# Kernel tuning notes

Measured on AMD Instinct MI355X. Metric: run time of the kernel, lower is better.

Reference implementation:

```python
import jax, jax.numpy as jnp
import numpy as np

EMBED_DIM = 1024
N_HEADS = 16
HEAD_DIM = EMBED_DIM // N_HEADS


def setup_inputs() -> dict:
    key = jax.random.key(0)
    k1, k2, k3 = jax.random.split(key, 3)
    B, T, C = 2, 2048, EMBED_DIM
    x = jax.random.normal(k1, (B, T, C), dtype=jnp.float32)
    # nn.Linear-style init scale
    s = 1.0 / np.sqrt(C)
    Wqkv = jax.random.normal(k2, (C, 3 * C), dtype=jnp.float32) * s
    bqkv = jnp.zeros((3 * C,), dtype=jnp.float32)
    Wout = jax.random.normal(k3, (C, C), dtype=jnp.float32) * s
    bout = jnp.zeros((C,), dtype=jnp.float32)
    return {"x": x, "Wqkv": Wqkv, "bqkv": bqkv, "Wout": Wout, "bout": bout}


def reference(x, Wqkv, bqkv, Wout, bout):
    B, T, C = x.shape
    H, D = N_HEADS, HEAD_DIM
    qkv = x @ Wqkv + bqkv  # [B,T,3C]
    q, k, v = jnp.split(qkv, 3, axis=-1)
    # [B,T,C] -> [B,H,T,D]
    q = q.reshape(B, T, H, D).transpose(0, 2, 1, 3)
    k = k.reshape(B, T, H, D).transpose(0, 2, 1, 3)
    v = v.reshape(B, T, H, D).transpose(0, 2, 1, 3)
    scale = 1.0 / np.sqrt(D)
    scores = jnp.einsum("bhqd,bhkd->bhqk", q, k) * scale  # [B,H,T,T]
    causal = jnp.tril(jnp.ones((T, T), dtype=bool))  # True where allowed
    scores = jnp.where(causal, scores, jnp.finfo(scores.dtype).min)
    attn = jax.nn.softmax(scores, axis=-1)
    out = jnp.einsum("bhqk,bhkd->bhqd", attn, v)  # [B,H,T,D]
    out = out.transpose(0, 2, 1, 3).reshape(B, T, C)
    return out @ Wout + bout
```

## Files before the change

kernel.cpp:

```cpp
#include <hip/hip_runtime.h>
#include <hip/hip_bf16.h>
#include <stdint.h>

#define EMBED 1024
#define NH 16
#define HD 64
#define BATCH 2
#define SEQ 2048
#define MTOK (BATCH*SEQ)

using bf8 = __attribute__((ext_vector_type(8))) short;
using f4  = __attribute__((ext_vector_type(4))) float;
using f16v = __attribute__((ext_vector_type(16))) float;
using u16x4 = __attribute__((ext_vector_type(4))) unsigned short;

union U4 { uint32_t u[4]; bf8 v; };

__device__ __forceinline__ uint32_t pk_bf16(float a, float b) {
  __hip_bfloat162 h = __float22bfloat162_rn(float2{a, b});
  union { __hip_bfloat162 h; uint32_t u; } c; c.h = h; return c.u;
}
__device__ __forceinline__ unsigned short bfbits(float f) {
  __hip_bfloat16 h = __float2bfloat16(f);
  union { __hip_bfloat16 h; unsigned short u; } c; c.h = h; return c.u;
}
__device__ __forceinline__ float bf2f(unsigned short u) {
  union { uint32_t u; float f; } c; c.u = (uint32_t)u << 16; return c.f;
}
__device__ __forceinline__ float fexp2(float x) {
#if __has_builtin(__builtin_amdgcn_exp2f)
  return __builtin_amdgcn_exp2f(x);
#else
  return exp2f(x);
#endif
}
__device__ __forceinline__ float frcp(float x) {
#if __has_builtin(__builtin_amdgcn_rcpf)
  return __builtin_amdgcn_rcpf(x);
#else
  return 1.f / x;
#endif
}

__device__ __forceinline__ void gl2lds16(const void* g, void* l) {
  __builtin_amdgcn_global_load_lds(
      (const __attribute__((address_space(1))) void*)g,
      (__attribute__((address_space(3))) void*)l, 16, 0, 0);
}

__global__ __launch_bounds__(256) void prep(const float* __restrict__ x,
                                            unsigned short* __restrict__ xb,
                                            const float* __restrict__ Wqkv,
                                            unsigned short* __restrict__ wqkvT,
                                            const float* __restrict__ Wout,
                                            unsigned short* __restrict__ woutT) {
  __shared__ float tl[64][65];
  int blk = blockIdx.x;
  if (blk < 4096) {
    int i = (blk * 256 + threadIdx.x) * 4;
    float4 v = *(const float4*)(x + i);
    uint2 o;
    o.x = pk_bf16(v.x, v.y);
    o.y = pk_bf16(v.z, v.w);
    *(uint2*)(xb + i) = o;
    return;
  }
  const float* W; unsigned short* Wt; int K, N, bx, by;
  if (blk < 4096 + 768) {
    int j = blk - 4096; W = Wqkv; Wt = wqkvT; K = 1024; N = 3072;
    bx = j % 48; by = j / 48;
  } else {
    int j = blk - 4096 - 768; W = Wout; Wt = woutT; K = 1024; N = 1024;
    bx = j % 16; by = j / 16;
  }
  int k0 = by * 64, n0 = bx * 64;
  int tr = threadIdx.x >> 6, tc = threadIdx.x & 63;
#pragma unroll
  for (int i = 0; i < 16; i++) {
    int r = tr + i * 4;
    tl[r][tc] = W[(size_t)(k0 + r) * N + n0 + tc];
  }
  __syncthreads();
#pragma unroll
  for (int i = 0; i < 16; i++) {
    int r = tr + i * 4;
    Wt[(size_t)(n0 + r) * K + k0 + tc] = bfbits(tl[tc][r]);
  }
}

template<int BN, int MODE>
__global__ __launch_bounds__(256) void gemm_bt(const unsigned short* __restrict__ A,
                                               const unsigned short* __restrict__ Bt,
                                               const float* __restrict__ bias,
                                               unsigned short* __restrict__ Oq,
                                               unsigned short* __restrict__ Ov,
                                               float* __restrict__ Of,
                                               int M, int N, int K) {
  constexpr int MT = (BN == 128) ? 4 : 2;
  constexpr int BB = BN * 128;
  const int tid = threadIdx.x;
  const int w = tid >> 6, lane = tid & 63;
  const int wm = (BN == 128) ? (w >> 1) : w;
  const int wn = (BN == 128) ? (w & 1) : 0;
  const int m0 = blockIdx.y * 128, n0 = blockIdx.x * BN;

  __shared__ char smem[32768 + 2 * BB];

  f4 acc[MT][4] = {};

  auto STAGE = [&](int buf, int kk) {
    int k0 = kk * 64;
#pragma unroll
    for (int i = 0; i < 4; i++) {
      int c = i * 4 + w;
      int row = c * 8 + (lane >> 3);
      int col = ((lane & 7) * 8) ^ ((row & 7) << 3);
      gl2lds16(A + (size_t)(m0 + row) * K + k0 + col, smem + buf * 16384 + c * 1024);
    }
#pragma unroll
    for (int i = 0; i < BN / 32; i++) {
      int c = i * 4 + w;
      int row = c * 8 + (lane >> 3);
      int col = ((lane & 7) * 8) ^ ((row & 7) << 3);
      gl2lds16(Bt + (size_t)(n0 + row) * K + k0 + col, smem + 32768 + buf * BB + c * 1024);
    }
  };

  const int nk = K / 64;
  STAGE(0, 0);
  STAGE(1, 1);

  for (int kk = 0; kk < nk; kk++) {
    if (kk + 1 < nk) {
      if constexpr (BN == 128) { asm volatile("s_waitcnt vmcnt(8)" ::: "memory"); }
      else                     { asm volatile("s_waitcnt vmcnt(6)" ::: "memory"); }
    } else {
      asm volatile("s_waitcnt vmcnt(0)" ::: "memory");
    }
    __builtin_amdgcn_s_barrier();

    const char* Al = smem + (kk & 1) * 16384;
    const char* Bl = smem + 32768 + (kk & 1) * BB;
    __builtin_amdgcn_s_setprio(1);
#pragma unroll
    for (int ks = 0; ks < 2; ks++) {
      bf8 af[MT], bfr[4];
#pragma unroll
      for (int mt = 0; mt < MT; mt++) {
        int rr = wm * (MT * 16) + mt * 16 + (lane & 15);
        af[mt] = *(const bf8*)(Al + rr * 128 + ((ks * 64 + (lane >> 4) * 16) ^ ((rr & 7) << 4)));
      }
#pragma unroll
      for (int nt = 0; nt < 4; nt++) {
        int rr = wn * 64 + nt * 16 + (lane & 15);
        bfr[nt] = *(const bf8*)(Bl + rr * 128 + ((ks * 64 + (lane >> 4) * 16) ^ ((rr & 7) << 4)));
      }
#pragma unroll
      for (int mt = 0; mt < MT; mt++)
#pragma unroll
        for (int nt = 0; nt < 4; nt++)
          acc[mt][nt] = __builtin_amdgcn_mfma_f32_16x16x32_bf16(af[mt], bfr[nt], acc[mt][nt], 0, 0, 0);
    }
    __builtin_amdgcn_s_setprio(0);

    __builtin_amdgcn_s_barrier();
    if (kk + 2 < nk) STAGE(kk & 1, kk + 2);
  }

  if (MODE == 0) {
    const int region = n0 >> 10;
    if (region < 2) {
      float sc = (region == 0) ? 0.180336880f : 1.0f;
#pragma unroll
      for (int nt = 0; nt < 4; nt++) {
        int n = n0 + wn * 64 + nt * 16 + (lane & 15);
        float bv = bias[n];
        int c = n & 1023, h = c >> 6, d = c & 63;
#pragma unroll
        for (int mt = 0; mt < MT; mt++) {
#pragma unroll
          for (int r = 0; r < 4; r++) {
            int m = m0 + wm * (MT * 16) + mt * 16 + (lane >> 4) * 4 + r;
            int b = m >> 11, t = m & 2047;
            size_t off = ((((size_t)region * 2 + b) * 16 + h) * 2048 + t) * 64 + d;
            Oq[off] = bfbits((acc[mt][nt][r] + bv) * sc);
          }
        }
      }
    } else {
#pragma unroll
      for (int nt = 0; nt < 4; nt++) {
        int n = n0 + wn * 64 + nt * 16 + (lane & 15);
        float bv = bias[n];
        int c = n & 1023, h = c >> 6, d = c & 63;
#pragma unroll
        for (int mt = 0; mt < MT; mt++) {
          int m = m0 + wm * (MT * 16) + mt * 16 + (lane >> 4) * 4;
          int b = m >> 11, t = m & 2047;
          size_t off = (((size_t)b * 16 + h) * 64 + d) * 2048 + t;
          u16x4 pk4;
#pragma unroll
          for (int r = 0; r < 4; r++) pk4[r] = bfbits(acc[mt][nt][r] + bv);
          *(u16x4*)(Ov + off) = pk4;
        }
      }
    }
  } else {
#pragma unroll
    for (int mt = 0; mt < MT; mt++) {
#pragma unroll
      for (int r = 0; r < 4; r++) {
        int m = m0 + wm * (MT * 16) + mt * 16 + (lane >> 4) * 4 + r;
#pragma unroll
        for (int nt = 0; nt < 4; nt++) {
          int n = n0 + wn * 64 + nt * 16 + (lane & 15);
          Of[(size_t)m * N + n] = acc[mt][nt][r] + bias[n];
        }
      }
    }
  }
}

__global__ __launch_bounds__(256) void attn12(const unsigned short* __restrict__ Qb,
                                              const unsigned short* __restrict__ Kb,
                                              const unsigned short* __restrict__ Vtb,
                                              unsigned short* __restrict__ Ob,
                                              unsigned short* __restrict__ partO,
                                              float* __restrict__ Lbuf) {
  static const signed char QTs[32] = {15,15,14,14,13,13,12,12,11,11,10,10,9,8,7,6,5,15,4,9,14,3,8,13,2,7,12,1,6,11,0,5};
  static const signed char TSs[32] = {0,11,0,11,0,11,0,11,0,11,0,11,0,0,0,0,0,22,0,11,22,0,11,22,0,11,22,0,11,22,0,11};
  static const signed char PS[32]  = {0,1,2,3,4,5,6,7,8,9,10,11,12,13,14,15,16,17,-1,18,19,-1,20,21,-1,22,23,-1,24,25,-1,26};
  const int idx = blockIdx.x;
  const int s = idx >> 5, bh = idx & 31;
  const int qt = QTs[s], ts = TSs[s];
  const int ntot = 2 * qt + 2;
  const int te = min(ts + 11, ntot);
  const int slot = PS[s];

  const int tid = threadIdx.x;
  const int w = tid >> 6, lane = tid & 63;
  const int hi = lane >> 5, q32 = lane & 31;

  __shared__ char smem[49152];

  const unsigned short* Qg  = Qb  + (size_t)bh * SEQ * HD;
  const unsigned short* Kg  = Kb  + (size_t)bh * SEQ * HD;
  const unsigned short* Vtg = Vtb + (size_t)bh * SEQ * HD;

  const int qbw  = qt * 128 + w * 32;
  const int qrow = qbw + q32;

  bf8 qf[4];
#pragma unroll
  for (int kc = 0; kc < 4; kc++)
    qf[kc] = *(const bf8*)(Qg + (size_t)qrow * HD + kc * 16 + hi * 8);

  f16v acc0 = {}, acc1 = {};
  float lr = 0.f;

  auto STAGE = [&](int buf, int t) {
    int kv0 = t * 64;
#pragma unroll
    for (int i = 0; i < 2; i++) {
      int c = i * 4 + w;
      int row = c * 8 + (lane >> 3);
      int col = ((lane & 7) * 8) ^ ((row & 7) << 3);
      gl2lds16(Kg + (size_t)(kv0 + row) * HD + col,    smem + buf * 8192 + c * 1024);
      gl2lds16(Vtg + (size_t)row * SEQ + kv0 + col,    smem + 24576 + buf * 8192 + c * 1024);
    }
  };

  const int nt_loc = te - ts;
  STAGE(0, ts);
  if (nt_loc > 1) STAGE(1, ts + 1);

  for (int tl = 0; tl < nt_loc; tl++) {
    const int t = ts + tl;
    const int kv0 = t * 64;

    if (tl + 1 < nt_loc) {
      asm volatile("s_waitcnt vmcnt(4)" ::: "memory");
    } else {
      asm volatile("s_waitcnt vmcnt(0)" ::: "memory");
    }
    __builtin_amdgcn_s_barrier();
    if (tl + 2 < nt_loc) STAGE((tl + 2) % 3, t + 2);

    if (kv0 <= qbw + 31) {
      const char* kl = smem + (tl % 3) * 8192;
      const char* vl = smem + 24576 + (tl % 3) * 8192;
      const bool hi_vis = (kv0 + 32 <= qbw + 31);

      f16v s0 = {}, s1 = {};
      __builtin_amdgcn_s_setprio(1);
#pragma unroll
      for (int kc = 0; kc < 4; kc++) {
        int r0 = q32;
        bf8 k0 = *(const bf8*)(kl + r0 * 128 + ((kc * 32 + hi * 16) ^ ((r0 & 7) << 4)));
        s0 = __builtin_amdgcn_mfma_f32_32x32x16_bf16(k0, qf[kc], s0, 0, 0, 0);
      }
      if (hi_vis) {
#pragma unroll
        for (int kc = 0; kc < 4; kc++) {
          int r1 = 32 + q32;
          bf8 k1 = *(const bf8*)(kl + r1 * 128 + ((kc * 32 + hi * 16) ^ ((r1 & 7) << 4)));
          s1 = __builtin_amdgcn_mfma_f32_32x32x16_bf16(k1, qf[kc], s1, 0, 0, 0);
        }
      }
      __builtin_amdgcn_s_setprio(0);

      if (kv0 + 63 > qbw) {
#pragma unroll
        for (int r = 0; r < 16; r++) {
          int key = kv0 + (r & 3) + 8 * (r >> 2) + 4 * hi;
          if (key > qrow)      s0[r] = -1e30f;
          if (key + 32 > qrow) s1[r] = -1e30f;
        }
      }

      uint32_t u[16];
#pragma unroll
      for (int m8 = 0; m8 < 8; m8++) {
        float pa = fexp2(s0[2 * m8]), pb = fexp2(s0[2 * m8 + 1]);
        lr += pa + pb;
        u[m8] = pk_bf16(pa, pb);
      }
      if (hi_vis) {
#pragma unroll
        for (int m8 = 0; m8 < 8; m8++) {
          float pc = fexp2(s1[2 * m8]), pd = fexp2(s1[2 * m8 + 1]);
          lr += pc + pd;
          u[8 + m8] = pk_bf16(pc, pd);
        }
      }

      __builtin_amdgcn_s_setprio(1);
      const int ncc = hi_vis ? 4 : 2;
      for (int kcc = 0; kcc < ncc; kcc++) {
        const int base = (kcc >> 1) * 8 + (kcc & 1) * 4;
        uint32_t a0 = u[base + 0], a2 = u[base + 2];
        uint32_t a1 = u[base + 1], a3 = u[base + 3];
        asm("v_permlane32_swap_b32 %0, %1" : "+v"(a0), "+v"(a2));
        asm("v_permlane32_swap_b32 %0, %1" : "+v"(a1), "+v"(a3));
        U4 f; f.u[0] = a0; f.u[1] = a1; f.u[2] = a2; f.u[3] = a3;
        int r0 = q32, r1 = 32 + q32;
        bf8 v0 = *(const bf8*)(vl + r0 * 128 + ((kcc * 32 + hi * 16) ^ ((r0 & 7) << 4)));
        bf8 v1 = *(const bf8*)(vl + r1 * 128 + ((kcc * 32 + hi * 16) ^ ((r1 & 7) << 4)));
        acc0 = __builtin_amdgcn_mfma_f32_32x32x16_bf16(f.v, v0, acc0, 0, 0, 0);
        acc1 = __builtin_amdgcn_mfma_f32_32x32x16_bf16(f.v, v1, acc1, 0, 0, 0);
      }
      __builtin_amdgcn_s_setprio(0);
    }
  }

  lr += __shfl_xor(lr, 32);
  if (slot < 0) {
    int b = bh >> 4, h = bh & 15;
    unsigned short* Og = Ob + (size_t)b * SEQ * EMBED;
#pragma unroll
    for (int r = 0; r < 16; r++) {
      int ql_ = (r & 3) + 8 * (r >> 2) + 4 * hi;
      float linv = frcp(__shfl(lr, ql_));
      size_t rowoff = (size_t)(qbw + ql_) * EMBED + h * 64;
      Og[rowoff + q32]      = bfbits(acc0[r] * linv);
      Og[rowoff + 32 + q32] = bfbits(acc1[r] * linv);
    }
  } else {
    int pidx = slot * 32 + bh;
    unsigned short* P0 = partO + (size_t)pidx * 8192;
#pragma unroll
    for (int r = 0; r < 16; r++) {
      int ql_ = (r & 3) + 8 * (r >> 2) + 4 * hi;
      int rowl = w * 32 + ql_;
      P0[rowl * 64 + q32]      = bfbits(acc0[r]);
      P0[rowl * 64 + 32 + q32] = bfbits(acc1[r]);
    }
    if (hi == 0) Lbuf[pidx * 128 + w * 32 + q32] = lr;
  }
}

__global__ __launch_bounds__(256) void attn_combine(const unsigned short* __restrict__ partO,
                                                    const float* __restrict__ Lbuf,
                                                    unsigned short* __restrict__ Ob) {
  static const signed char NSg[11] = {2,2,2,2,2,2,3,3,3,3,3};
  static const signed char SL[11][3] = {
    {16,26,0},{15,24,0},{14,22,0},{13,20,0},{12,18,0},{10,11,0},
    {8,9,25},{6,7,23},{4,5,21},{2,3,19},{0,1,17}};
  int pair = blockIdx.x;
  int qi = pair >> 5, bh = pair & 31;
  int qt = 5 + qi;
  int ns = NSg[qi];
  int b = bh >> 4, h = bh & 15;
#pragma unroll
  for (int rr = 0; rr < 2; rr++) {
    int row = rr * 64 + (threadIdx.x >> 2);
    int d0 = (threadIdx.x & 3) * 16;
    float lsum = 0.f;
    float acc[16] = {};
    for (int sg = 0; sg < ns; sg++) {
      int pidx = (int)SL[qi][sg] * 32 + bh;
      lsum += Lbuf[pidx * 128 + row];
      const unsigned short* O0 = partO + (size_t)pidx * 8192 + row * 64 + d0;
#pragma unroll
      for (int v = 0; v < 4; v++) {
        u16x4 a = *(const u16x4*)(O0 + v * 4);
#pragma unroll
        for (int e = 0; e < 4; e++) acc[v * 4 + e] += bf2f(a[e]);
      }
    }
    float linv = 1.f / lsum;
    unsigned short* out = Ob + ((size_t)b * SEQ + qt * 128 + row) * EMBED + h * 64 + d0;
    u16x4 res[4];
#pragma unroll
    for (int v = 0; v < 4; v++) {
#pragma unroll
      for (int e = 0; e < 4; e++) res[v][e] = bfbits(acc[v * 4 + e] * linv);
    }
    *(u16x4*)(out)      = res[0];
    *(u16x4*)(out + 4)  = res[1];
    *(u16x4*)(out + 8)  = res[2];
    *(u16x4*)(out + 12) = res[3];
  }
}

extern "C" void kernel_launch(void* const* d_in, const int* in_sizes, int n_in,
                              void* d_out, int out_size, void* d_ws, size_t ws_size,
                              hipStream_t stream) {
  const float* x    = (const float*)d_in[0];
  const float* Wqkv = (const float*)d_in[1];
  const float* bqkv = (const float*)d_in[2];
  const float* Wout = (const float*)d_in[3];
  const float* bout = (const float*)d_in[4];
  float* out = (float*)d_out;

  char* ws = (char*)d_ws;
  unsigned short* xb    = (unsigned short*)ws;
  unsigned short* wqkvT = (unsigned short*)(ws + (size_t)8 * 1048576);
  unsigned short* partO = (unsigned short*)ws;
  float*          lbuf  = (float*)(ws + 14155776);
  unsigned short* woutT = (unsigned short*)(ws + (size_t)14 * 1048576);
  unsigned short* qk    = (unsigned short*)(ws + (size_t)16 * 1048576);
  unsigned short* vT    = (unsigned short*)(ws + (size_t)32 * 1048576);
  unsigned short* obuf  = (unsigned short*)(ws + (size_t)40 * 1048576);

  prep<<<dim3(4096 + 768 + 256), 256, 0, stream>>>(x, xb, Wqkv, wqkvT, Wout, woutT);

  gemm_bt<128, 0><<<dim3(24, 32), 256, 0, stream>>>(xb, wqkvT, bqkv, qk, vT, nullptr,
                                                    MTOK, 3 * EMBED, EMBED);

  const unsigned short* Qb = qk;
  const unsigned short* Kb = qk + (size_t)BATCH * NH * SEQ * HD;
  attn12<<<dim3(32 * 32), 256, 0, stream>>>(Qb, Kb, vT, obuf, partO, lbuf);
  attn_combine<<<dim3(11 * 32), 256, 0, stream>>>(partO, lbuf, obuf);

  gemm_bt<128, 1><<<dim3(8, 32), 256, 0, stream>>>(obuf, woutT, bout, nullptr, nullptr, out,
                                                   MTOK, EMBED, EMBED);
}
```

Before: 104.6 us.

## Replace QKV projection GEMM with 256x256-tile 8-wave pipelined kernel

```diff
diff --git a/kernel.cpp b/kernel.cpp
--- a/kernel.cpp
+++ b/kernel.cpp
@@ -88,6 +88,152 @@
   }
 }
 
+__global__ __launch_bounds__(512, 2) void gemm8(const unsigned short* __restrict__ A,
+                                                const unsigned short* __restrict__ Bt,
+                                                const float* __restrict__ bias,
+                                                unsigned short* __restrict__ Oq,
+                                                unsigned short* __restrict__ Ov,
+                                                int M, int N, int K) {
+  const int tid = threadIdx.x;
+  const int w = tid >> 6, lane = tid & 63;
+  const int wm = w >> 2, wn = w & 3;
+  const int m0 = blockIdx.y * 256, n0 = blockIdx.x * 256;
+
+  __shared__ char smem[131072];
+
+  f4 acc[8][4] = {};
+
+  auto stA = [&](int buf, int kk, int ca) {
+    int row = ca * 8 + (lane >> 3);
+    int col = ((lane & 7) * 8) ^ ((row & 7) << 3);
+    gl2lds16(A + (size_t)(m0 + row) * K + kk * 64 + col, smem + buf * 32768 + ca * 1024);
+  };
+  auto stB = [&](int buf, int kk, int cb) {
+    int row = cb * 8 + (lane >> 3);
+    int col = ((lane & 7) * 8) ^ ((row & 7) << 3);
+    gl2lds16(Bt + (size_t)(n0 + row) * K + kk * 64 + col, smem + 65536 + buf * 32768 + cb * 1024);
+  };
+
+  const int nk = K / 64;
+#pragma unroll
+  for (int c = 0; c < 4; c++) stA(0, 0, c * 8 + w);
+#pragma unroll
+  for (int c = 0; c < 4; c++) stB(0, 0, c * 8 + w);
+#pragma unroll
+  for (int c = 0; c < 4; c++) stA(1, 1, c * 8 + w);
+#pragma unroll
+  for (int c = 0; c < 4; c++) stB(1, 1, c * 8 + w);
+
+  for (int T = 0; T < nk; T++) {
+    const int buf = T & 1;
+    const char* Al = smem + buf * 32768;
+    const char* Bl = smem + 65536 + buf * 32768;
+
+    if (T + 1 < nk) { asm volatile("s_waitcnt vmcnt(7)" ::: "memory"); }
+    else            { asm volatile("s_waitcnt vmcnt(0)" ::: "memory"); }
+    __builtin_amdgcn_s_barrier();
+    if (T >= 1 && T + 1 < nk) {
+      int ca = (w < 4) ? (12 + w) : (24 + w);
+      stA((T + 1) & 1, T + 1, ca);
+    }
+    bf8 bfrag[4][2];
+#pragma unroll
+    for (int nt = 0; nt < 4; nt++) {
+      int rr = wn * 64 + nt * 16 + (lane & 15);
+#pragma unroll
+      for (int ks = 0; ks < 2; ks++)
+        bfrag[nt][ks] = *(const bf8*)(Bl + rr * 128 + ((ks * 64 + (lane >> 4) * 16) ^ ((rr & 7) << 4)));
+    }
+    {
+      bf8 af[2][2];
+#pragma unroll
+      for (int i = 0; i < 2; i++) {
+        int rr = wm * 128 + i * 16 + (lane & 15);
+#pragma unroll
+        for (int ks = 0; ks < 2; ks++)
+          af[i][ks] = *(const bf8*)(Al + rr * 128 + ((ks * 64 + (lane >> 4) * 16) ^ ((rr & 7) << 4)));
+      }
+      __builtin_amdgcn_s_setprio(1);
+#pragma unroll
+      for (int i = 0; i < 2; i++)
+#pragma unroll
+        for (int nt = 0; nt < 4; nt++)
+#pragma unroll
+          for (int ks = 0; ks < 2; ks++)
+            acc[i][nt] = __builtin_amdgcn_mfma_f32_16x16x32_bf16(af[i][ks], bfrag[nt][ks], acc[i][nt], 0, 0, 0);
+      __builtin_amdgcn_s_setprio(0);
+    }
+    __builtin_amdgcn_s_barrier();
+
+#pragma unroll
+    for (int p = 1; p < 4; p++) {
+      if (T + 2 < nk) {
+        int ca = (w < 4) ? (4 * (p - 1) + w) : (16 + 4 * (p - 1) + (w - 4));
+        stA(buf, T + 2, ca);
+        if (p == 1)      { stB(buf, T + 2, w * 2); stB(buf, T + 2, w * 2 + 1); }
+        else if (p == 2) { stB(buf, T + 2, 16 + w); }
+        else             { stB(buf, T + 2, 24 + w); }
+      }
+      bf8 af[2][2];
+#pragma unroll
+      for (int i = 0; i < 2; i++) {
+        int rr = wm * 128 + (2 * p + i) * 16 + (lane & 15);
+#pragma unroll
+        for (int ks = 0; ks < 2; ks++)
+          af[i][ks] = *(const bf8*)(Al + rr * 128 + ((ks * 64 + (lane >> 4) * 16) ^ ((rr & 7) << 4)));
+      }
+      __builtin_amdgcn_s_setprio(1);
+#pragma unroll
+      for (int i = 0; i < 2; i++)
+#pragma unroll
+        for (int nt = 0; nt < 4; nt++)
+#pragma unroll
+          for (int ks = 0; ks < 2; ks++)
+            acc[2 * p + i][nt] = __builtin_amdgcn_mfma_f32_16x16x32_bf16(af[i][ks], bfrag[nt][ks], acc[2 * p + i][nt], 0, 0, 0);
+      __builtin_amdgcn_s_setprio(0);
+      __builtin_amdgcn_s_barrier();
+    }
+  }
+
+  const int region = n0 >> 10;
+  if (region < 2) {
+    float sc = (region == 0) ? 0.180336880f : 1.0f;
+#pragma unroll
+    for (int nt = 0; nt < 4; nt++) {
+      int n = n0 + wn * 64 + nt * 16 + (lane & 15);
+      float bv = bias[n];
+      int c = n & 1023, h = c >> 6, d = c & 63;
+#pragma unroll
+      for (int mf = 0; mf < 8; mf++) {
+#pragma unroll
+        for (int r = 0; r < 4; r++) {
+          int m = m0 + wm * 128 + mf * 16 + (lane >> 4) * 4 + r;
+          int b = m >> 11, t = m & 2047;
+          size_t off = ((((size_t)region * 2 + b) * 16 + h) * 2048 + t) * 64 + d;
+          Oq[off] = bfbits((acc[mf][nt][r] + bv) * sc);
+        }
+      }
+    }
+  } else {
+#pragma unroll
+    for (int nt = 0; nt < 4; nt++) {
+      int n = n0 + wn * 64 + nt * 16 + (lane & 15);
+      float bv = bias[n];
+      int c = n & 1023, h = c >> 6, d = c & 63;
+#pragma unroll
+      for (int mf = 0; mf < 8; mf++) {
+        int m = m0 + wm * 128 + mf * 16 + (lane >> 4) * 4;
+        int b = m >> 11, t = m & 2047;
+        size_t off = (((size_t)b * 16 + h) * 64 + d) * 2048 + t;
+        u16x4 pk4;
+#pragma unroll
+        for (int r = 0; r < 4; r++) pk4[r] = bfbits(acc[mf][nt][r] + bv);
+        *(u16x4*)(Ov + off) = pk4;
+      }
+    }
+  }
+}
+
 template<int BN, int MODE>
 __global__ __launch_bounds__(256) void gemm_bt(const unsigned short* __restrict__ A,
                                                const unsigned short* __restrict__ Bt,
@@ -445,8 +591,7 @@
 
   prep<<<dim3(4096 + 768 + 256), 256, 0, stream>>>(x, xb, Wqkv, wqkvT, Wout, woutT);
 
-  gemm_bt<128, 0><<<dim3(24, 32), 256, 0, stream>>>(xb, wqkvT, bqkv, qk, vT, nullptr,
-                                                    MTOK, 3 * EMBED, EMBED);
+  gemm8<<<dim3(12, 16), 512, 0, stream>>>(xb, wqkvT, bqkv, qk, vT, MTOK, 3 * EMBED, EMBED);
 
   const unsigned short* Qb = qk;
   const unsigned short* Kb = qk + (size_t)BATCH * NH * SEQ * HD;
```

Measured after the change: 109.7 us. 4.8% more time.
